# Kernel tuning notes

Hardware: AMD Instinct MI355X
Metric: run time of the kernel (lower is better)

The kernel has to match this reference:

```python
import jax, jax.numpy as jnp
import numpy as np

T, N, E = 512, 64, 1024   # encoder frames, batch, encoder feature dim
H = 320                   # pred_hidden_size
J = 512                   # joint hidden
V = 29                    # vocab incl. blank
BLANK = V - 1
MAX_SYM = 30              # max_symbols_per_step


def setup_inputs() -> dict:
    key = jax.random.key(0)
    ks = jax.random.split(key, 16)
    sH = 1.0 / np.sqrt(H)
    sE = 1.0 / np.sqrt(E)
    sJ = 1.0 / np.sqrt(J)
    b_o = jax.random.normal(ks[14], (V,), jnp.float32) * 0.1
    b_o = b_o.at[BLANK].add(4.0)  # blank-dominant logits -> realistic sparse emissions
    return {
        "f": jax.random.normal(ks[0], (T, N, E), jnp.float32),
        "f_lens": jax.random.randint(ks[1], (N,), T // 2, T + 1).astype(jnp.int32),
        "emb": jax.random.normal(ks[2], (V - 1, H), jnp.float32) * 0.1,
        "wi0": jax.random.normal(ks[3], (4 * H, H), jnp.float32) * sH,
        "wh0": jax.random.normal(ks[4], (4 * H, H), jnp.float32) * sH,
        "bi0": jax.random.normal(ks[5], (4 * H,), jnp.float32) * 0.05,
        "bh0": jax.random.normal(ks[6], (4 * H,), jnp.float32) * 0.05,
        "wi1": jax.random.normal(ks[7], (4 * H, H), jnp.float32) * sH,
        "wh1": jax.random.normal(ks[8], (4 * H, H), jnp.float32) * sH,
        "bi1": jax.random.normal(ks[9], (4 * H,), jnp.float32) * 0.05,
        "bh1": jax.random.normal(ks[10], (4 * H,), jnp.float32) * 0.05,
        "w_f": jax.random.normal(ks[11], (J, E), jnp.float32) * sE,
        "w_g": jax.random.normal(ks[12], (J, H), jnp.float32) * sH,
        "b_j": jax.random.normal(ks[13], (J,), jnp.float32) * 0.05,
        "w_o": jax.random.normal(ks[15], (V, J), jnp.float32) * sJ,
        "b_o": b_o,
    }


def reference(f, f_lens, emb, wi0, wh0, bi0, bh0, wi1, wh1, bi1, bh1,
              w_f, w_g, b_j, w_o, b_o):
    n = f.shape[1]
    rows = jnp.arange(n)

    def cell(x, h, c, wi, wh, bi, bh):
        g = x @ wi.T + h @ wh.T + (bi + bh)
        i, fg, gg, o = jnp.split(g, 4, axis=-1)  # torch LSTM gate order i,f,g,o
        c2 = jax.nn.sigmoid(fg) * c + jax.nn.sigmoid(i) * jnp.tanh(gg)
        return jax.nn.sigmoid(o) * jnp.tanh(c2), c2

    def pred_step(last_sym, h, c):
        # SOS (=-1) embeds to zeros
        x = jnp.where(last_sym[:, None] < 0, 0.0, emb[jnp.clip(last_sym, 0, V - 2)])
        h0, c0 = cell(x, h[0], c[0], wi0, wh0, bi0, bh0)
        h1, c1 = cell(h0, h[1], c[1], wi1, wh1, bi1, bh1)
        return h1, jnp.stack([h0, h1]), jnp.stack([c0, c1])

    def joint(fi, g):
        hj = jax.nn.relu(fi @ w_f.T + g @ w_g.T + b_j)
        return hj @ w_o.T + b_o

    def cond(st):
        return jnp.any(st[0] < f_lens)

    def body(st):
        time_idx, sym_add, res, res_idx, last, h, c = st
        fi = f[jnp.clip(time_idx, 0, T - 1), rows]            # [N,E] per-element frame
        g, h_new, c_new = pred_step(last, h, c)               # one LSTM step
        sym = jnp.argmax(joint(fi, g), axis=1).astype(jnp.int32)
        active = time_idx < f_lens
        emit = active & (sym != BLANK) & (sym_add < MAX_SYM)
        adv = active & ~emit                                   # blank or symbol cap -> advance time
        slot = jnp.where(emit, res_idx + 1, 0)
        res = res.at[rows, slot].set(jnp.where(emit, sym, res[rows, slot]))
        res_idx = res_idx + emit.astype(jnp.int32)
        sym_add = jnp.where(emit, sym_add + 1, jnp.where(adv, 0, sym_add))
        time_idx = time_idx + adv.astype(jnp.int32)
        last = jnp.where(emit, sym, last)
        m = emit[None, :, None]
        return (time_idx, sym_add, res, res_idx, last,
                jnp.where(m, h_new, h), jnp.where(m, c_new, c))

    init = (jnp.zeros((n,), jnp.int32),                        # time_idx
            jnp.zeros((n,), jnp.int32),                        # symbols_added
            jnp.full((n, MAX_SYM * T), -1, jnp.int32),         # res
            jnp.full((n,), -1, jnp.int32),                     # res_idx
            jnp.full((n,), -1, jnp.int32),                     # pred_g (SOS)
            jnp.zeros((2, n, H), jnp.float32),                 # pred h
            jnp.zeros((2, n, H), jnp.float32))                 # pred c
    st = jax.lax.while_loop(cond, body, init)
    res, res_idx = st[2], st[3]
    return res, res_idx + 1
```

## Files before the change

kernel.cpp:

```cpp
#include <hip/hip_runtime.h>
#include <math.h>

#define T_ 512
#define N_ 64
#define E_ 1024
#define H_ 320
#define HS8_ 40
#define J_ 512
#define V_ 29
#define BLANK_ 28
#define MAXSYM_ 30
#define RESW_ (MAXSYM_ * T_)

__device__ float g_Xi0[V_][4 * H_];
__device__ float g_b1s[4 * H_];
__device__ float g_h0x[2][N_][H_];
__device__ float g_h1x[2][N_][H_];
__device__ float g_gpx[2][N_][8][J_];
__device__ unsigned int g_flag[N_];

#define BM_ 128
#define BN_ 128
#define BK_ 16

__global__ __launch_bounds__(256) void fproj_gemm(
    const float* __restrict__ A, const float* __restrict__ B,
    const float* __restrict__ bj, float* __restrict__ C) {
  __shared__ __align__(16) float As[BK_][BM_ + 4];
  __shared__ __align__(16) float Bs[BK_][BN_ + 4];
  const int tid = threadIdx.x;
  const int m0 = blockIdx.x * BM_;
  const int j0 = blockIdx.y * BN_;
  const int tx = tid & 15, ty = tid >> 4;
  const int sm = tid >> 1;
  const int sk = (tid & 1) << 3;

  float acc[8][8];
#pragma unroll
  for (int i = 0; i < 8; ++i)
#pragma unroll
    for (int j = 0; j < 8; ++j) acc[i][j] = 0.f;

  for (int kc = 0; kc < E_; kc += BK_) {
    float4 av0 = *(const float4*)(A + (size_t)(m0 + sm) * E_ + kc + sk);
    float4 av1 = *(const float4*)(A + (size_t)(m0 + sm) * E_ + kc + sk + 4);
    float4 bv0 = *(const float4*)(B + (size_t)(j0 + sm) * E_ + kc + sk);
    float4 bv1 = *(const float4*)(B + (size_t)(j0 + sm) * E_ + kc + sk + 4);
    __syncthreads();
    As[sk + 0][sm] = av0.x; As[sk + 1][sm] = av0.y;
    As[sk + 2][sm] = av0.z; As[sk + 3][sm] = av0.w;
    As[sk + 4][sm] = av1.x; As[sk + 5][sm] = av1.y;
    As[sk + 6][sm] = av1.z; As[sk + 7][sm] = av1.w;
    Bs[sk + 0][sm] = bv0.x; Bs[sk + 1][sm] = bv0.y;
    Bs[sk + 2][sm] = bv0.z; Bs[sk + 3][sm] = bv0.w;
    Bs[sk + 4][sm] = bv1.x; Bs[sk + 5][sm] = bv1.y;
    Bs[sk + 6][sm] = bv1.z; Bs[sk + 7][sm] = bv1.w;
    __syncthreads();
#pragma unroll
    for (int k = 0; k < BK_; ++k) {
      float a_[8], b_[8];
      *(float4*)&a_[0] = *(const float4*)&As[k][ty * 8];
      *(float4*)&a_[4] = *(const float4*)&As[k][ty * 8 + 4];
      *(float4*)&b_[0] = *(const float4*)&Bs[k][tx * 8];
      *(float4*)&b_[4] = *(const float4*)&Bs[k][tx * 8 + 4];
#pragma unroll
      for (int i = 0; i < 8; ++i)
#pragma unroll
        for (int j = 0; j < 8; ++j) acc[i][j] += a_[i] * b_[j];
    }
  }

#pragma unroll
  for (int i = 0; i < 8; ++i) {
    const size_t m = (size_t)(m0 + ty * 8 + i);
#pragma unroll
    for (int j = 0; j < 8; j += 4) {
      float4 v;
      v.x = acc[i][j + 0] + bj[j0 + tx * 8 + j + 0];
      v.y = acc[i][j + 1] + bj[j0 + tx * 8 + j + 1];
      v.z = acc[i][j + 2] + bj[j0 + tx * 8 + j + 2];
      v.w = acc[i][j + 3] + bj[j0 + tx * 8 + j + 3];
      *(float4*)(C + m * J_ + j0 + tx * 8 + j) = v;
    }
  }
}

__global__ void init_kernel(int* __restrict__ res) {
  const int idx = blockIdx.x * blockDim.x + threadIdx.x;
  if (idx < N_) g_flag[idx] = 0u;
  const int stride = gridDim.x * blockDim.x;
  for (size_t i = idx; i < (size_t)N_ * RESW_; i += stride) res[i] = -1;
}

__global__ __launch_bounds__(256) void xi0_kernel(
    const float* __restrict__ emb, const float* __restrict__ wi0,
    const float* __restrict__ bi0, const float* __restrict__ bh0,
    const float* __restrict__ bi1, const float* __restrict__ bh1) {
  __shared__ __align__(16) float xs[H_];
  const int s = blockIdx.x;
  const int tid = threadIdx.x;
  for (int i = tid; i < H_; i += 256)
    xs[i] = (s < V_ - 1) ? emb[(size_t)s * H_ + i] : 0.f;
  __syncthreads();
  for (int o = tid; o < 4 * H_; o += 256) {
    float acc = bi0[o] + bh0[o];
    if (s < V_ - 1) {
      const float* wr = wi0 + (size_t)o * H_;
      for (int k = 0; k < H_; k += 4) {
        float4 x4 = *(const float4*)&xs[k];
        float4 w4 = *(const float4*)&wr[k];
        acc += x4.x * w4.x + x4.y * w4.y + x4.z * w4.z + x4.w * w4.w;
      }
    }
    g_Xi0[s][o] = acc;
    if (s == 0) g_b1s[o] = bi1[o] + bh1[o];
  }
}

__device__ __forceinline__ float sigmoidf_(float x) {
  return 1.f / (1.f + expf(-x));
}

__device__ __forceinline__ void flag_round8(int row, int tid, int& target) {
  target += 8;
  __syncthreads();
  if (tid == 0) {
    __hip_atomic_fetch_add(&g_flag[row], 1u, __ATOMIC_RELEASE,
                           __HIP_MEMORY_SCOPE_AGENT);
    while (__hip_atomic_load(&g_flag[row], __ATOMIC_ACQUIRE,
                             __HIP_MEMORY_SCOPE_AGENT) < (unsigned)target)
      __builtin_amdgcn_s_sleep(2);
  }
  __syncthreads();
}

__device__ void recompute8(
    int s, int row, int k8, int tid, int par, int& target,
    const float* __restrict__ wh0, const float* __restrict__ wi1,
    const float* __restrict__ wh1, const float* __restrict__ w_g,
    float* h0s, float* h1s, float* gates,
    float& c0, float& c1, float2& gp) {
  const int g = tid / HS8_;
  const int il = tid - g * HS8_;
  const int o = g * H_ + k8 * HS8_ + il;

  if (tid < 4 * HS8_) {
    const float* wr = wh0 + (size_t)o * H_;
    float acc = g_Xi0[s][o];
    for (int kk = 0; kk < H_; kk += 4) {
      float4 h4 = *(const float4*)&h0s[kk];
      float4 w4 = *(const float4*)&wr[kk];
      acc += h4.x * w4.x + h4.y * w4.y + h4.z * w4.z + h4.w * w4.w;
    }
    gates[tid] = acc;
  }
  __syncthreads();
  if (tid < HS8_) {
    float ig = sigmoidf_(gates[tid]);
    float fg = sigmoidf_(gates[HS8_ + tid]);
    float gg = tanhf(gates[2 * HS8_ + tid]);
    float og = sigmoidf_(gates[3 * HS8_ + tid]);
    float c2 = fg * c0 + ig * gg;
    c0 = c2;
    float h2 = og * tanhf(c2);
    __hip_atomic_store(&g_h0x[par][row][k8 * HS8_ + tid], h2, __ATOMIC_RELAXED,
                       __HIP_MEMORY_SCOPE_AGENT);
  }
  float acc1 = 0.f;
  if (tid < 4 * HS8_) {
    const float* whr = wh1 + (size_t)o * H_;
    acc1 = g_b1s[o];
    for (int kk = 0; kk < H_; kk += 4) {
      float4 h4 = *(const float4*)&h1s[kk];
      float4 w4 = *(const float4*)&whr[kk];
      acc1 += h4.x * w4.x + h4.y * w4.y + h4.z * w4.z + h4.w * w4.w;
    }
  }
  flag_round8(row, tid, target);
  h0s[tid] = __hip_atomic_load(&g_h0x[par][row][tid], __ATOMIC_RELAXED,
                               __HIP_MEMORY_SCOPE_AGENT);
  if (tid < H_ - 256)
    h0s[256 + tid] = __hip_atomic_load(&g_h0x[par][row][256 + tid],
                                       __ATOMIC_RELAXED, __HIP_MEMORY_SCOPE_AGENT);
  __syncthreads();
  if (tid < 4 * HS8_) {
    const float* wir = wi1 + (size_t)o * H_;
    for (int kk = 0; kk < H_; kk += 4) {
      float4 x4 = *(const float4*)&h0s[kk];
      float4 w4 = *(const float4*)&wir[kk];
      acc1 += x4.x * w4.x + x4.y * w4.y + x4.z * w4.z + x4.w * w4.w;
    }
    gates[tid] = acc1;
  }
  __syncthreads();
  if (tid < HS8_) {
    float ig = sigmoidf_(gates[tid]);
    float fg = sigmoidf_(gates[HS8_ + tid]);
    float gg = tanhf(gates[2 * HS8_ + tid]);
    float og = sigmoidf_(gates[3 * HS8_ + tid]);
    float c2 = fg * c1 + ig * gg;
    c1 = c2;
    float h2 = og * tanhf(c2);
    h1s[k8 * HS8_ + tid] = h2;
    __hip_atomic_store(&g_h1x[par][row][k8 * HS8_ + tid], h2, __ATOMIC_RELAXED,
                       __HIP_MEMORY_SCOPE_AGENT);
  }
  __syncthreads();
  {
    const float* hsl = &h1s[k8 * HS8_];
#pragma unroll
    for (int jj = 0; jj < 2; ++jj) {
      const int j = tid + jj * 256;
      const float* wgr = w_g + (size_t)j * H_ + k8 * HS8_;
      float a = 0.f;
      for (int kk = 0; kk < HS8_; kk += 4) {
        float4 h4 = *(const float4*)&hsl[kk];
        float4 w4 = *(const float4*)&wgr[kk];
        a += h4.x * w4.x + h4.y * w4.y + h4.z * w4.z + h4.w * w4.w;
      }
      __hip_atomic_store(&g_gpx[par][row][k8][j], a, __ATOMIC_RELAXED,
                         __HIP_MEMORY_SCOPE_AGENT);
    }
  }
  flag_round8(row, tid, target);
  {
    float ax = 0.f, ay = 0.f;
#pragma unroll
    for (int kk = 0; kk < 8; ++kk) {
      ax += __hip_atomic_load(&g_gpx[par][row][kk][2 * tid], __ATOMIC_RELAXED,
                              __HIP_MEMORY_SCOPE_AGENT);
      ay += __hip_atomic_load(&g_gpx[par][row][kk][2 * tid + 1], __ATOMIC_RELAXED,
                              __HIP_MEMORY_SCOPE_AGENT);
    }
    gp.x = ax; gp.y = ay;
  }
  h1s[tid] = __hip_atomic_load(&g_h1x[par][row][tid], __ATOMIC_RELAXED,
                               __HIP_MEMORY_SCOPE_AGENT);
  if (tid < H_ - 256)
    h1s[256 + tid] = __hip_atomic_load(&g_h1x[par][row][256 + tid],
                                       __ATOMIC_RELAXED, __HIP_MEMORY_SCOPE_AGENT);
  __syncthreads();
}

__global__ __launch_bounds__(256, 2) void decode8(
    const float* __restrict__ Fproj, const int* __restrict__ f_lens,
    const float* __restrict__ wh0,
    const float* __restrict__ wi1, const float* __restrict__ wh1,
    const float* __restrict__ w_g,
    const float* __restrict__ w_o, const float* __restrict__ b_o,
    int* __restrict__ res, int* __restrict__ nsym) {
  const int bid = blockIdx.x;
  const int k8 = bid & 7;
  const int row = ((bid >> 3) + 8 * k8) & 63;
  const int tid = threadIdx.x;
  const int f_len = f_lens[row];

  __shared__ __align__(16) float h0s[H_], h1s[H_];
  __shared__ __align__(16) float gates[4 * HS8_];
  __shared__ __align__(16) float hjs[J_];
  __shared__ float logits[32];

  const int v = tid >> 3;
  const int lq = tid & 7;
  float4 wo[16];
  float bo = 0.f;
  if (v < V_) {
#pragma unroll
    for (int q = 0; q < 16; ++q)
      wo[q] = *(const float4*)(w_o + (size_t)v * J_ + lq * 4 + 32 * q);
    bo = b_o[v];
  }

  for (int i = tid; i < H_; i += 256) { h0s[i] = 0.f; h1s[i] = 0.f; }
  float c0 = 0.f, c1 = 0.f;
  float2 gp = {0.f, 0.f};
  int target = 0;
  __syncthreads();

  recompute8(BLANK_, row, k8, tid, 0, target, wh0, wi1, wh1, w_g,
             h0s, h1s, gates, c0, c1, gp);
  int ecount = 1;

  int t_loc = 0, sym_add = 0, res_idx = -1;
  float2 fp = *(const float2*)(Fproj + (size_t)row * J_ + 2 * tid);

  while (t_loc < f_len) {
    const int tn = (t_loc + 1 < T_) ? t_loc + 1 : T_ - 1;
    float2 fpn = *(const float2*)(Fproj + ((size_t)tn * N_ + row) * J_ + 2 * tid);

    float hx = fp.x + gp.x, hy = fp.y + gp.y;
    float2 hj2 = {hx > 0.f ? hx : 0.f, hy > 0.f ? hy : 0.f};
    *(float2*)&hjs[2 * tid] = hj2;
    __syncthreads();

    float p = 0.f;
    if (v < V_) {
#pragma unroll
      for (int q = 0; q < 16; ++q) {
        float4 h4 = *(const float4*)&hjs[lq * 4 + 32 * q];
        p += h4.x * wo[q].x + h4.y * wo[q].y + h4.z * wo[q].z + h4.w * wo[q].w;
      }
    }
    p += __shfl_xor(p, 4, 8);
    p += __shfl_xor(p, 2, 8);
    p += __shfl_xor(p, 1, 8);
    if (v < V_ && lq == 0) logits[v] = p + bo;
    __syncthreads();

    float best = logits[0];
    int bi = 0;
#pragma unroll
    for (int vv = 1; vv < V_; ++vv) {
      float lv = logits[vv];
      if (lv > best) { best = lv; bi = vv; }
    }
    const int emit = (bi != BLANK_) && (sym_add < MAXSYM_);

    if (emit) {
      res_idx += 1;
      if (k8 == 0 && tid == 0) res[(size_t)row * RESW_ + res_idx] = bi;
      sym_add += 1;
      recompute8(bi, row, k8, tid, ecount & 1, target, wh0, wi1, wh1, w_g,
                 h0s, h1s, gates, c0, c1, gp);
      ecount += 1;
    } else {
      sym_add = 0;
      t_loc += 1;
      fp = fpn;
    }
  }

  if (k8 == 0 && tid == 0) nsym[row] = res_idx + 1;
}

extern "C" void kernel_launch(void* const* d_in, const int* in_sizes, int n_in,
                              void* d_out, int out_size, void* d_ws, size_t ws_size,
                              hipStream_t stream) {
  const float* f      = (const float*)d_in[0];
  const int*   f_lens = (const int*)d_in[1];
  const float* emb    = (const float*)d_in[2];
  const float* wi0    = (const float*)d_in[3];
  const float* wh0    = (const float*)d_in[4];
  const float* bi0    = (const float*)d_in[5];
  const float* bh0    = (const float*)d_in[6];
  const float* wi1    = (const float*)d_in[7];
  const float* wh1    = (const float*)d_in[8];
  const float* bi1    = (const float*)d_in[9];
  const float* bh1    = (const float*)d_in[10];
  const float* w_f    = (const float*)d_in[11];
  const float* w_g    = (const float*)d_in[12];
  const float* b_j    = (const float*)d_in[13];
  const float* w_o    = (const float*)d_in[14];
  const float* b_o    = (const float*)d_in[15];

  int* out  = (int*)d_out;
  int* res  = out;
  int* nsym = out + (size_t)N_ * RESW_;

  float* Fproj = (float*)d_ws;

  init_kernel<<<1024, 256, 0, stream>>>(res);
  xi0_kernel<<<V_, 256, 0, stream>>>(emb, wi0, bi0, bh0, bi1, bh1);

  dim3 ggrid(T_ * N_ / BM_, J_ / BN_);
  fproj_gemm<<<ggrid, 256, 0, stream>>>(f, w_f, b_j, Fproj);

  decode8<<<N_ * 8, 256, 0, stream>>>(Fproj, f_lens, wh0, wi1, wh1, w_g,
                                      w_o, b_o, res, nsym);
}
```

Baseline: 1.996 ms.

## Batch joint over four frames, merge setup kernels, pad GEMM smem, shorten spin sleep

The decode loop now evaluates the joint network for four consecutive frames at once, because the prediction state only changes on emission. It then scans the four results for the first emitting frame, so runs of blanks cost one pass of barriers instead of four. The init, Xi0 and GEMM launches are merged into one kernel, the B tile in shared memory gets a padded layout, and the spin-wait sleep is shortened. The batched joint wastes work on the frames after an emission, which are recomputed on the next pass.

```diff
diff --git a/kernel.cpp b/kernel.cpp
--- a/kernel.cpp
+++ b/kernel.cpp
@@ -12,6 +12,11 @@
 #define MAXSYM_ 30
 #define RESW_ (MAXSYM_ * T_)
 
+#define BM_ 128
+#define BN_ 128
+#define BK_ 16
+#define GEMMB_ 1024
+
 __device__ float g_Xi0[V_][4 * H_];
 __device__ float g_b1s[4 * H_];
 __device__ float g_h0x[2][N_][H_];
@@ -19,21 +24,60 @@
 __device__ float g_gpx[2][N_][8][J_];
 __device__ unsigned int g_flag[N_];
 
-#define BM_ 128
-#define BN_ 128
-#define BK_ 16
-
-__global__ __launch_bounds__(256) void fproj_gemm(
+#define BSW_ 144
+__device__ __forceinline__ int padcol(int c) { return c + ((c >> 5) << 2); }
+
+__global__ __launch_bounds__(256) void gemm_init_kernel(
     const float* __restrict__ A, const float* __restrict__ B,
-    const float* __restrict__ bj, float* __restrict__ C) {
+    const float* __restrict__ bj, float* __restrict__ C,
+    const float* __restrict__ emb, const float* __restrict__ wi0,
+    const float* __restrict__ bi0, const float* __restrict__ bh0,
+    const float* __restrict__ bi1, const float* __restrict__ bh1,
+    int* __restrict__ res) {
+  const int bid = blockIdx.x;
+  const int tid = threadIdx.x;
+
+  if (bid >= GEMMB_) {
+    const int ab = bid - GEMMB_;
+    if (ab < V_) {
+      __shared__ __align__(16) float xs[H_];
+      for (int i = tid; i < H_; i += 256)
+        xs[i] = (ab < V_ - 1) ? emb[(size_t)ab * H_ + i] : 0.f;
+      __syncthreads();
+      for (int o = tid; o < 4 * H_; o += 256) {
+        float acc = bi0[o] + bh0[o];
+        if (ab < V_ - 1) {
+          const float* wr = wi0 + (size_t)o * H_;
+          for (int k = 0; k < H_; k += 4) {
+            float4 x4 = *(const float4*)&xs[k];
+            float4 w4 = *(const float4*)&wr[k];
+            acc += x4.x * w4.x + x4.y * w4.y + x4.z * w4.z + x4.w * w4.w;
+          }
+        }
+        g_Xi0[ab][o] = acc;
+        if (ab == 0) g_b1s[o] = bi1[o] + bh1[o];
+      }
+    } else {
+      if (ab == V_ && tid < N_) g_flag[tid] = 0u;
+      const int fb = ab - V_;
+      int4* r4 = (int4*)res;
+      const size_t tot = (size_t)N_ * RESW_ / 4;
+      const size_t i0 = (size_t)fb * 256 + tid;
+      const int4 mval = {-1, -1, -1, -1};
+      for (size_t i = i0; i < tot; i += 3 * 256) r4[i] = mval;
+    }
+    return;
+  }
+
   __shared__ __align__(16) float As[BK_][BM_ + 4];
-  __shared__ __align__(16) float Bs[BK_][BN_ + 4];
-  const int tid = threadIdx.x;
-  const int m0 = blockIdx.x * BM_;
-  const int j0 = blockIdx.y * BN_;
+  __shared__ __align__(16) float Bs[BK_][BSW_];
+  const int m0 = blockIdx.x / 4 * BM_;
+  const int j0 = (blockIdx.x & 3) * BN_;
   const int tx = tid & 15, ty = tid >> 4;
   const int sm = tid >> 1;
   const int sk = (tid & 1) << 3;
+  const int smP = padcol(sm);
+  const int bcol = padcol(tx * 8);
 
   float acc[8][8];
 #pragma unroll
@@ -51,18 +95,18 @@
     As[sk + 2][sm] = av0.z; As[sk + 3][sm] = av0.w;
     As[sk + 4][sm] = av1.x; As[sk + 5][sm] = av1.y;
     As[sk + 6][sm] = av1.z; As[sk + 7][sm] = av1.w;
-    Bs[sk + 0][sm] = bv0.x; Bs[sk + 1][sm] = bv0.y;
-    Bs[sk + 2][sm] = bv0.z; Bs[sk + 3][sm] = bv0.w;
-    Bs[sk + 4][sm] = bv1.x; Bs[sk + 5][sm] = bv1.y;
-    Bs[sk + 6][sm] = bv1.z; Bs[sk + 7][sm] = bv1.w;
+    Bs[sk + 0][smP] = bv0.x; Bs[sk + 1][smP] = bv0.y;
+    Bs[sk + 2][smP] = bv0.z; Bs[sk + 3][smP] = bv0.w;
+    Bs[sk + 4][smP] = bv1.x; Bs[sk + 5][smP] = bv1.y;
+    Bs[sk + 6][smP] = bv1.z; Bs[sk + 7][smP] = bv1.w;
     __syncthreads();
 #pragma unroll
     for (int k = 0; k < BK_; ++k) {
       float a_[8], b_[8];
       *(float4*)&a_[0] = *(const float4*)&As[k][ty * 8];
       *(float4*)&a_[4] = *(const float4*)&As[k][ty * 8 + 4];
-      *(float4*)&b_[0] = *(const float4*)&Bs[k][tx * 8];
-      *(float4*)&b_[4] = *(const float4*)&Bs[k][tx * 8 + 4];
+      *(float4*)&b_[0] = *(const float4*)&Bs[k][bcol];
+      *(float4*)&b_[4] = *(const float4*)&Bs[k][bcol + 4];
 #pragma unroll
       for (int i = 0; i < 8; ++i)
 #pragma unroll
@@ -85,38 +129,6 @@
   }
 }
 
-__global__ void init_kernel(int* __restrict__ res) {
-  const int idx = blockIdx.x * blockDim.x + threadIdx.x;
-  if (idx < N_) g_flag[idx] = 0u;
-  const int stride = gridDim.x * blockDim.x;
-  for (size_t i = idx; i < (size_t)N_ * RESW_; i += stride) res[i] = -1;
-}
-
-__global__ __launch_bounds__(256) void xi0_kernel(
-    const float* __restrict__ emb, const float* __restrict__ wi0,
-    const float* __restrict__ bi0, const float* __restrict__ bh0,
-    const float* __restrict__ bi1, const float* __restrict__ bh1) {
-  __shared__ __align__(16) float xs[H_];
-  const int s = blockIdx.x;
-  const int tid = threadIdx.x;
-  for (int i = tid; i < H_; i += 256)
-    xs[i] = (s < V_ - 1) ? emb[(size_t)s * H_ + i] : 0.f;
-  __syncthreads();
-  for (int o = tid; o < 4 * H_; o += 256) {
-    float acc = bi0[o] + bh0[o];
-    if (s < V_ - 1) {
-      const float* wr = wi0 + (size_t)o * H_;
-      for (int k = 0; k < H_; k += 4) {
-        float4 x4 = *(const float4*)&xs[k];
-        float4 w4 = *(const float4*)&wr[k];
-        acc += x4.x * w4.x + x4.y * w4.y + x4.z * w4.z + x4.w * w4.w;
-      }
-    }
-    g_Xi0[s][o] = acc;
-    if (s == 0) g_b1s[o] = bi1[o] + bh1[o];
-  }
-}
-
 __device__ __forceinline__ float sigmoidf_(float x) {
   return 1.f / (1.f + expf(-x));
 }
@@ -129,7 +141,7 @@
                            __HIP_MEMORY_SCOPE_AGENT);
     while (__hip_atomic_load(&g_flag[row], __ATOMIC_ACQUIRE,
                              __HIP_MEMORY_SCOPE_AGENT) < (unsigned)target)
-      __builtin_amdgcn_s_sleep(2);
+      __builtin_amdgcn_s_sleep(1);
   }
   __syncthreads();
 }
@@ -257,8 +269,8 @@
 
   __shared__ __align__(16) float h0s[H_], h1s[H_];
   __shared__ __align__(16) float gates[4 * HS8_];
-  __shared__ __align__(16) float hjs[J_];
-  __shared__ float logits[32];
+  __shared__ __align__(16) float hjs[4][J_];
+  __shared__ float logits[4][32];
 
   const int v = tid >> 3;
   const int lq = tid & 7;
@@ -282,51 +294,70 @@
   int ecount = 1;
 
   int t_loc = 0, sym_add = 0, res_idx = -1;
-  float2 fp = *(const float2*)(Fproj + (size_t)row * J_ + 2 * tid);
 
   while (t_loc < f_len) {
-    const int tn = (t_loc + 1 < T_) ? t_loc + 1 : T_ - 1;
-    float2 fpn = *(const float2*)(Fproj + ((size_t)tn * N_ + row) * J_ + 2 * tid);
-
-    float hx = fp.x + gp.x, hy = fp.y + gp.y;
-    float2 hj2 = {hx > 0.f ? hx : 0.f, hy > 0.f ? hy : 0.f};
-    *(float2*)&hjs[2 * tid] = hj2;
+    float2 fp[4];
+#pragma unroll
+    for (int b = 0; b < 4; ++b) {
+      const int tb = (t_loc + b < T_) ? t_loc + b : T_ - 1;
+      fp[b] = *(const float2*)(Fproj + ((size_t)tb * N_ + row) * J_ + 2 * tid);
+    }
+#pragma unroll
+    for (int b = 0; b < 4; ++b) {
+      float hx = fp[b].x + gp.x, hy = fp[b].y + gp.y;
+      hjs[b][2 * tid] = hx > 0.f ? hx : 0.f;
+      hjs[b][2 * tid + 1] = hy > 0.f ? hy : 0.f;
+    }
     __syncthreads();
 
-    float p = 0.f;
+    float pb[4] = {0.f, 0.f, 0.f, 0.f};
     if (v < V_) {
 #pragma unroll
       for (int q = 0; q < 16; ++q) {
-        float4 h4 = *(const float4*)&hjs[lq * 4 + 32 * q];
-        p += h4.x * wo[q].x + h4.y * wo[q].y + h4.z * wo[q].z + h4.w * wo[q].w;
+        const int c = lq * 4 + 32 * q;
+        const float4 w4 = wo[q];
+#pragma unroll
+        for (int b = 0; b < 4; ++b) {
+          float4 h4 = *(const float4*)&hjs[b][c];
+          pb[b] += h4.x * w4.x + h4.y * w4.y + h4.z * w4.z + h4.w * w4.w;
+        }
       }
     }
-    p += __shfl_xor(p, 4, 8);
-    p += __shfl_xor(p, 2, 8);
-    p += __shfl_xor(p, 1, 8);
-    if (v < V_ && lq == 0) logits[v] = p + bo;
+#pragma unroll
+    for (int b = 0; b < 4; ++b) {
+      pb[b] += __shfl_xor(pb[b], 4, 8);
+      pb[b] += __shfl_xor(pb[b], 2, 8);
+      pb[b] += __shfl_xor(pb[b], 1, 8);
+    }
+    if (v < V_ && lq == 0) {
+#pragma unroll
+      for (int b = 0; b < 4; ++b) logits[b][v] = pb[b] + bo;
+    }
     __syncthreads();
 
-    float best = logits[0];
-    int bi = 0;
-#pragma unroll
-    for (int vv = 1; vv < V_; ++vv) {
-      float lv = logits[vv];
-      if (lv > best) { best = lv; bi = vv; }
-    }
-    const int emit = (bi != BLANK_) && (sym_add < MAXSYM_);
-
-    if (emit) {
-      res_idx += 1;
-      if (k8 == 0 && tid == 0) res[(size_t)row * RESW_ + res_idx] = bi;
-      sym_add += 1;
-      recompute8(bi, row, k8, tid, ecount & 1, target, wh0, wi1, wh1, w_g,
-                 h0s, h1s, gates, c0, c1, gp);
-      ecount += 1;
-    } else {
+    int emit_sym = -1;
+#pragma unroll 1
+    for (int b = 0; b < 4; ++b) {
+      float best = logits[b][0];
+      int bi = 0;
+#pragma unroll
+      for (int vv = 1; vv < V_; ++vv) {
+        float lv = logits[b][vv];
+        if (lv > best) { best = lv; bi = vv; }
+      }
+      if ((bi != BLANK_) && (sym_add < MAXSYM_)) { emit_sym = bi; break; }
       sym_add = 0;
       t_loc += 1;
-      fp = fpn;
+      if (t_loc >= f_len) break;
+    }
+
+    if (emit_sym >= 0) {
+      res_idx += 1;
+      if (k8 == 0 && tid == 0) res[(size_t)row * RESW_ + res_idx] = emit_sym;
+      sym_add += 1;
+      recompute8(emit_sym, row, k8, tid, ecount & 1, target, wh0, wi1, wh1,
+                 w_g, h0s, h1s, gates, c0, c1, gp);
+      ecount += 1;
     }
   }
 
@@ -359,11 +390,8 @@
 
   float* Fproj = (float*)d_ws;
 
-  init_kernel<<<1024, 256, 0, stream>>>(res);
-  xi0_kernel<<<V_, 256, 0, stream>>>(emb, wi0, bi0, bh0, bi1, bh1);
-
-  dim3 ggrid(T_ * N_ / BM_, J_ / BN_);
-  fproj_gemm<<<ggrid, 256, 0, stream>>>(f, w_f, b_j, Fproj);
+  gemm_init_kernel<<<GEMMB_ + 32, 256, 0, stream>>>(
+      f, w_f, b_j, Fproj, emb, wi0, bi0, bh0, bi1, bh1, res);
 
   decode8<<<N_ * 8, 256, 0, stream>>>(Fproj, f_lens, wh0, wi1, wh1, w_g,
                                       w_o, b_o, res, nsym);
```

Result: slower. 2.839 ms (+42.2%).
